# Kernel optimization log

Measured on AMD Instinct MI355X. Metric: run time of the kernel, lower is better.

The kernel has to match this reference:

```python
import jax, jax.numpy as jnp
import numpy as np

LN_EPS = 1e-5

def layer_norm(x, w, b):
    mu = jnp.mean(x, axis=-1, keepdims=True)
    var = jnp.mean(jnp.square(x - mu), axis=-1, keepdims=True)
    return (x - mu) * jax.lax.rsqrt(var + LN_EPS) * w + b

def setup_inputs() -> dict:
    key = jax.random.key(0)
    ks = jax.random.split(key, 8)
    B, F, Q, D = 8, 4096, 64, 1024
    H, DH = 16, 64
    inner = H * DH
    s = 1.0 / np.sqrt(D)
    return {
        "features": jax.random.normal(ks[0], (B, F, D), jnp.float32),
        "latents": jax.random.normal(ks[1], (B, Q, D), jnp.float32),
        "key_attention_mask": jax.random.randint(ks[2], (B, F), 0, 2, jnp.int32),
        "ln_m_w": jnp.ones((D,), jnp.float32),
        "ln_m_b": jnp.zeros((D,), jnp.float32),
        "ln_l_w": jnp.ones((D,), jnp.float32),
        "ln_l_b": jnp.zeros((D,), jnp.float32),
        "Wq": jax.random.normal(ks[3], (D, inner), jnp.float32) * s,
        "Wk": jax.random.normal(ks[4], (D, inner), jnp.float32) * s,
        "Wv": jax.random.normal(ks[5], (D, inner), jnp.float32) * s,
        "Wo": jax.random.normal(ks[6], (inner, D), jnp.float32) * (1.0 / np.sqrt(inner)),
    }

def reference(features, latents, key_attention_mask, ln_m_w, ln_m_b, ln_l_w, ln_l_b, Wq, Wk, Wv, Wo):
    H, DH = 16, 64
    B, F, D = features.shape
    Q = latents.shape[1]
    scale = DH ** (-0.5)

    x = layer_norm(features, ln_m_w, ln_m_b)          # [B,F,D]
    lat = layer_norm(latents, ln_l_w, ln_l_b)          # [B,Q,D]

    q = (lat @ Wq).reshape(B, Q, H, DH).transpose(0, 2, 1, 3)   # [B,H,Q,DH]
    kv_in = jnp.concatenate([x, lat], axis=1)                    # [B,F+Q,D]
    k = (kv_in @ Wk).reshape(B, F + Q, H, DH).transpose(0, 2, 1, 3)
    v = (kv_in @ Wv).reshape(B, F + Q, H, DH).transpose(0, 2, 1, 3)

    q = q * scale
    sim = jnp.einsum('bhqd,bhfd->bhqf', q, k)                    # [B,H,Q,F+Q]

    full_mask = jnp.concatenate(
        [key_attention_mask, jnp.ones((B, Q), key_attention_mask.dtype)], axis=1)  # [B,F+Q]
    sim = jnp.where(full_mask[:, None, None, :] == 0, -jnp.inf, sim)

    sim = sim - jax.lax.stop_gradient(jnp.max(sim, axis=-1, keepdims=True))
    alphas = jax.nn.softmax(sim, axis=-1)
    out = jnp.einsum('bhqf,bhfv->bhqv', alphas, v)               # [B,H,Q,DH]
    out = out.transpose(0, 2, 1, 3).reshape(B, Q, H * DH)        # [B,Q,inner]
    return out @ Wo                                              # [B,Q,D]
```

## Files before the change

### kernel.cpp

```cpp
#include <hip/hip_runtime.h>
#include <hip/hip_bf16.h>

#define B_    8
#define F_    4096
#define Qn    64
#define Dm    1024
#define Hh    16
#define DHn   64
#define FQ    4160
#define ROWS_KV 33280
#define ROWS_F  32768
#define KS    13
#define CHPB  5
#define KVOFF ((size_t)ROWS_KV * 1024)

typedef __bf16 v8bf __attribute__((ext_vector_type(8)));
typedef __bf16 v4bf __attribute__((ext_vector_type(4)));
typedef float  v4f  __attribute__((ext_vector_type(4)));

__device__ inline void gl_lds16(const __bf16* g, __bf16* l) {
  __builtin_amdgcn_global_load_lds((__attribute__((address_space(1))) void*)(g),
                                   (__attribute__((address_space(3))) void*)(l),
                                   16, 0, 0);
}

__device__ inline bool is_bf16_inputs(const void* mw) {
  return ((const unsigned int*)mw)[0] != 0x3F800000u;
}

__global__ __launch_bounds__(256) void transpose_kernel(
    const void* __restrict__ w0, const void* __restrict__ w1,
    const void* __restrict__ w2, const void* __restrict__ w3,
    __bf16* __restrict__ t0, __bf16* __restrict__ t1,
    __bf16* __restrict__ t2, __bf16* __restrict__ t3,
    const void* __restrict__ mw)
{
  bool bf = is_bf16_inputs(mw);
  __shared__ __bf16 tile[32][33];
  const void* src; __bf16* dst;
  switch (blockIdx.z) {
    case 0: src = w0; dst = t0; break;
    case 1: src = w1; dst = t1; break;
    case 2: src = w2; dst = t2; break;
    default: src = w3; dst = t3; break;
  }
  int tx = threadIdx.x, ty = threadIdx.y;
  int x = blockIdx.x * 32 + tx;
  #pragma unroll
  for (int j = 0; j < 4; ++j) {
    int y = blockIdx.y * 32 + ty + j * 8;
    size_t e = (size_t)y * 1024 + x;
    float v = bf ? (float)((const __bf16*)src)[e] : ((const float*)src)[e];
    tile[ty + j * 8][tx] = (__bf16)v;
  }
  __syncthreads();
  int x2 = blockIdx.y * 32 + tx;
  #pragma unroll
  for (int j = 0; j < 4; ++j) {
    int y2 = blockIdx.x * 32 + ty + j * 8;
    dst[(size_t)y2 * 1024 + x2] = tile[tx][ty + j * 8];
  }
}

__global__ __launch_bounds__(256) void ln_kernel(
    const void* __restrict__ feat, const void* __restrict__ lat,
    const void* __restrict__ mw, const void* __restrict__ mb,
    const void* __restrict__ lw, const void* __restrict__ lb,
    __bf16* __restrict__ kv_bf, __bf16* __restrict__ lat_bf)
{
  bool bf = is_bf16_inputs(mw);
  int tid = threadIdx.x;
  int wave = tid >> 6, lane = tid & 63;
  int r = blockIdx.x * 4 + wave;
  const void *rowp, *w, *g;
  __bf16 *dst, *dst2 = nullptr;
  size_t rowoff;
  if (r < ROWS_F) {
    rowoff = (size_t)r * Dm; rowp = feat; w = mw; g = mb;
    int b = r >> 12, f = r & (F_ - 1);
    dst = kv_bf + ((size_t)b * FQ + f) * Dm;
  } else {
    int r2 = r - ROWS_F;
    rowoff = (size_t)r2 * Dm; rowp = lat; w = lw; g = lb;
    int b = r2 >> 6, q = r2 & 63;
    dst  = kv_bf + ((size_t)b * FQ + F_ + q) * Dm;
    dst2 = lat_bf + (size_t)r2 * Dm;
  }
  float xs[16], ws_[16], gs[16];
  if (bf) {
    const __bf16* rp = (const __bf16*)rowp + rowoff;
    const __bf16* wp = (const __bf16*)w;
    const __bf16* gp = (const __bf16*)g;
    #pragma unroll
    for (int g2 = 0; g2 < 2; ++g2) {
      int base = g2 * 512 + lane * 8;
      v8bf X = *(const v8bf*)(rp + base);
      v8bf W = *(const v8bf*)(wp + base);
      v8bf G = *(const v8bf*)(gp + base);
      #pragma unroll
      for (int j = 0; j < 8; ++j) {
        xs[g2*8+j] = (float)X[j]; ws_[g2*8+j] = (float)W[j]; gs[g2*8+j] = (float)G[j];
      }
    }
  } else {
    const float* rp = (const float*)rowp + rowoff;
    const float* wp = (const float*)w;
    const float* gp = (const float*)g;
    #pragma unroll
    for (int g4 = 0; g4 < 4; ++g4) {
      int base = g4 * 256 + lane * 4;
      float4 X = *(const float4*)(rp + base);
      float4 W = *(const float4*)(wp + base);
      float4 G = *(const float4*)(gp + base);
      xs[g4*4]=X.x; xs[g4*4+1]=X.y; xs[g4*4+2]=X.z; xs[g4*4+3]=X.w;
      ws_[g4*4]=W.x; ws_[g4*4+1]=W.y; ws_[g4*4+2]=W.z; ws_[g4*4+3]=W.w;
      gs[g4*4]=G.x; gs[g4*4+1]=G.y; gs[g4*4+2]=G.z; gs[g4*4+3]=G.w;
    }
  }
  float s = 0.f, ss = 0.f;
  #pragma unroll
  for (int j = 0; j < 16; ++j) { s += xs[j]; ss += xs[j] * xs[j]; }
  #pragma unroll
  for (int off = 32; off > 0; off >>= 1) {
    s  += __shfl_xor(s, off, 64);
    ss += __shfl_xor(ss, off, 64);
  }
  float mean = s * (1.f / 1024.f);
  float var  = ss * (1.f / 1024.f) - mean * mean;
  float rs = rsqrtf(var + 1e-5f);
  float os[16];
  #pragma unroll
  for (int j = 0; j < 16; ++j) os[j] = (xs[j] - mean) * rs * ws_[j] + gs[j];
  if (bf) {
    #pragma unroll
    for (int g2 = 0; g2 < 2; ++g2) {
      int base = g2 * 512 + lane * 8;
      v8bf O;
      #pragma unroll
      for (int j = 0; j < 8; ++j) O[j] = (__bf16)os[g2*8+j];
      *(v8bf*)(dst + base) = O;
      if (dst2) *(v8bf*)(dst2 + base) = O;
    }
  } else {
    #pragma unroll
    for (int g4 = 0; g4 < 4; ++g4) {
      int base = g4 * 256 + lane * 4;
      v4bf O;
      #pragma unroll
      for (int j = 0; j < 4; ++j) O[j] = (__bf16)os[g4*4+j];
      *(v4bf*)(dst + base) = O;
      if (dst2) *(v4bf*)(dst2 + base) = O;
    }
  }
}


#define BAR() asm volatile("s_barrier" ::: "memory")

#define PH(Q) do { \
  BAR(); \
  asm volatile("s_waitcnt lgkmcnt(0)" ::: "memory"); \
  __builtin_amdgcn_s_setprio(1); \
  Q; \
  __builtin_amdgcn_s_setprio(0); \
  BAR(); \
} while (0)

#define PHV(Q) do { \
  BAR(); \
  asm volatile("s_waitcnt lgkmcnt(0)" ::: "memory"); \
  __builtin_amdgcn_s_setprio(1); \
  Q; \
  __builtin_amdgcn_s_setprio(0); \
  asm volatile("s_waitcnt vmcnt(4)" ::: "memory"); \
  BAR(); \
} while (0)

#define QUAD(MB, NB, BF) do { \
  _Pragma("unroll") \
  for (int m_ = 0; m_ < 4; ++m_) { \
    _Pragma("unroll") \
    for (int n_ = 0; n_ < 2; ++n_) { \
      _Pragma("unroll") \
      for (int k_ = 0; k_ < 2; ++k_) { \
        acc[(MB) + m_][(NB) + n_] = __builtin_amdgcn_mfma_f32_16x16x32_bf16( \
            af[m_][k_], BF[n_][k_], acc[(MB) + m_][(NB) + n_], 0, 0, 0); \
      } } } } while (0)

#define LDA8(BB, ROFF) do { \
  _Pragma("unroll") \
  for (int m_ = 0; m_ < 4; ++m_) { \
    _Pragma("unroll") \
    for (int k_ = 0; k_ < 2; ++k_) { \
      const int r_ = (ROFF) + m_ * 16 + lm; \
      af[m_][k_] = *(const v8bf*)(aB[BB] + ((r_ << 7) + ((k_ * 64 + kcb) ^ ((r_ & 7) << 4)))); \
    } } } while (0)

#define LDB4(BB, DST, NOFF) do { \
  _Pragma("unroll") \
  for (int n_ = 0; n_ < 2; ++n_) { \
    _Pragma("unroll") \
    for (int k_ = 0; k_ < 2; ++k_) { \
      const int r_ = bq + (NOFF) + n_ * 16 + lm; \
      DST[n_][k_] = *(const v8bf*)(bB[BB] + ((r_ << 7) + ((k_ * 64 + kcb) ^ ((r_ & 7) << 4)))); \
    } } } while (0)

#define STAGE_A(BB, H, K0) do { \
  gl_lds16(asrc + (size_t)(H) * 131072 + (K0),         (__bf16*)(ldsw + ((BB) * 4 + (H)) * 16384)); \
  gl_lds16(asrc + (size_t)(H) * 131072 + (K0) + 65536, (__bf16*)(ldsw + ((BB) * 4 + (H)) * 16384 + 8192)); \
} while (0)

#define STAGE_B(BB, H, K0) do { \
  gl_lds16(bsrc + (size_t)(H) * 131072 + (K0),         (__bf16*)(ldsw + ((BB) * 4 + 2 + (H)) * 16384)); \
  gl_lds16(bsrc + (size_t)(H) * 131072 + (K0) + 65536, (__bf16*)(ldsw + ((BB) * 4 + 2 + (H)) * 16384 + 8192)); \
} while (0)

__global__ __launch_bounds__(512, 2) void gemm_kv8_kernel(
    const __bf16* __restrict__ A, const __bf16* __restrict__ BtKV,
    __bf16* __restrict__ KVb)
{
  __shared__ __align__(16) char ldsm[131072];
  const int tid = threadIdx.x;
  const int lane = tid & 63, wave = tid >> 6;
  const int wm = wave >> 2, wn = wave & 3;
  const int lm = lane & 15, l4 = lane >> 4;
  const int kcb = l4 << 4;
  const int bq = (wn & 1) << 6;

  const int wg = (blockIdx.x & 7) * 130 + (blockIdx.x >> 3);
  const int n0 = (wg & 7) << 8;
  const int m0 = (wg >> 3) << 8;

  const int r0 = (wave << 3) + (lane >> 3);
  const int xc = ((lane & 7) ^ (lane >> 3)) << 3;
  const __bf16* asrc = A    + (size_t)(m0 + r0) * 1024 + xc;
  const __bf16* bsrc = BtKV + (size_t)(n0 + r0) * 1024 + xc;
  char* const ldsw = ldsm + tid * 16;
  const char* const aB[2] = { ldsm + wm * 16384, ldsm + (4 + wm) * 16384 };
  const char* const bB[2] = { ldsm + (2 + (wn >> 1)) * 16384,
                              ldsm + (6 + (wn >> 1)) * 16384 };

  v4f acc[8][4];
  #pragma unroll
  for (int i = 0; i < 8; ++i)
    #pragma unroll
    for (int j = 0; j < 4; ++j) acc[i][j] = (v4f){0.f, 0.f, 0.f, 0.f};
  v8bf af[4][2], blo[2][2], bhi[2][2];

  STAGE_A(0, 0, 0); STAGE_A(0, 1, 0);
  STAGE_B(0, 0, 0); STAGE_B(0, 1, 0);
  STAGE_B(1, 0, 64); STAGE_B(1, 1, 64);
  asm volatile("s_waitcnt vmcnt(4)" ::: "memory");
  BAR();

  #pragma unroll 1
  for (int it = 0; it < 8; ++it) {
    const int kA1 = (2 * it + 1) << 6;
    const int kT0 = (it < 7) ? ((2 * it + 2) << 6) : 0;
    const int kT1 = (it < 7) ? ((2 * it + 3) << 6) : 0;

    LDA8(0, 0); LDB4(0, blo, 0);
    STAGE_A(1, 0, kA1);
    PH(QUAD(0, 0, blo));

    LDB4(0, bhi, 32);
    STAGE_A(1, 1, kA1);
    PH(QUAD(0, 2, bhi));

    LDA8(0, 64);
    STAGE_B(0, 0, kT0);
    PH(QUAD(4, 2, bhi));

    STAGE_B(0, 1, kT0);
    PHV(QUAD(4, 0, blo));

    LDA8(1, 0); LDB4(1, blo, 0);
    STAGE_A(0, 0, kT0);
    PH(QUAD(0, 0, blo));

    LDB4(1, bhi, 32);
    STAGE_A(0, 1, kT0);
    PH(QUAD(0, 2, bhi));

    LDA8(1, 64);
    STAGE_B(1, 0, kT1);
    PH(QUAD(4, 2, bhi));

    STAGE_B(1, 1, kT1);
    PHV(QUAD(4, 0, blo));
  }

  const int cb = n0 + (wn << 6);
  const int rb = m0 + (wm << 7);
  #pragma unroll
  for (int m = 0; m < 8; ++m)
    #pragma unroll
    for (int n = 0; n < 4; ++n) {
      int col = cb + n * 16 + lm;
      int h = (col >> 6) & 15;
      int dh = col & 63;
      size_t vo = (col >= 1024) ? KVOFF : (size_t)0;
      #pragma unroll
      for (int reg = 0; reg < 4; ++reg) {
        int row = rb + m * 16 + l4 * 4 + reg;
        int bb2 = row / FQ; int f = row - bb2 * FQ;
        size_t idx = ((size_t)(bb2 * Hh + h) * FQ + f) * 64 + dh;
        KVb[idx + vo] = (__bf16)acc[m][n][reg];
      }
    }
}

__global__ __launch_bounds__(256) void gemm2_kernel(
    const __bf16* __restrict__ A, const __bf16* __restrict__ Bt,
    void* __restrict__ C, int mode, int out_follow,
    const void* __restrict__ mw)
{
  int obf = out_follow ? (is_bf16_inputs(mw) ? 1 : 0) : 1;

  __shared__ __align__(16) __bf16 As0[128 * 32];
  __shared__ __align__(16) __bf16 As1[128 * 32];
  __shared__ __align__(16) __bf16 Bs0[128 * 32];
  __shared__ __align__(16) __bf16 Bs1[128 * 32];
  int tid = threadIdx.x;
  int lane = tid & 63, wave = tid >> 6;
  int wm = wave >> 1, wn = wave & 1;
  int m0 = blockIdx.y * 128, n0 = blockIdx.x * 128;
  int lm = lane & 15, lk = (lane >> 4) << 3;

  v4f acc[4][4];
  #pragma unroll
  for (int i = 0; i < 4; ++i)
    #pragma unroll
    for (int j = 0; j < 4; ++j) acc[i][j] = (v4f){0.f, 0.f, 0.f, 0.f};

  int c0 = tid, c1 = tid + 256;
  const __bf16* a0p = A  + (size_t)(m0 + (c0 >> 2)) * 1024 + ((c0 & 3) << 3);
  const __bf16* a1p = A  + (size_t)(m0 + (c1 >> 2)) * 1024 + ((c1 & 3) << 3);
  const __bf16* b0p = Bt + (size_t)(n0 + (c0 >> 2)) * 1024 + ((c0 & 3) << 3);
  const __bf16* b1p = Bt + (size_t)(n0 + (c1 >> 2)) * 1024 + ((c1 & 3) << 3);

  for (int k0 = 0; k0 < 1024; k0 += 64) {
    __syncthreads();
    gl_lds16(a0p + k0,      &As0[c0 * 8]);
    gl_lds16(a1p + k0,      &As0[c1 * 8]);
    gl_lds16(a0p + k0 + 32, &As1[c0 * 8]);
    gl_lds16(a1p + k0 + 32, &As1[c1 * 8]);
    gl_lds16(b0p + k0,      &Bs0[c0 * 8]);
    gl_lds16(b1p + k0,      &Bs0[c1 * 8]);
    gl_lds16(b0p + k0 + 32, &Bs1[c0 * 8]);
    gl_lds16(b1p + k0 + 32, &Bs1[c1 * 8]);
    __syncthreads();
    {
      v8bf a[4], b[4];
      #pragma unroll
      for (int i = 0; i < 4; ++i) a[i] = *(const v8bf*)&As0[(wm * 64 + i * 16 + lm) * 32 + lk];
      #pragma unroll
      for (int j = 0; j < 4; ++j) b[j] = *(const v8bf*)&Bs0[(wn * 64 + j * 16 + lm) * 32 + lk];
      #pragma unroll
      for (int i = 0; i < 4; ++i)
        #pragma unroll
        for (int j = 0; j < 4; ++j)
          acc[i][j] = __builtin_amdgcn_mfma_f32_16x16x32_bf16(a[i], b[j], acc[i][j], 0, 0, 0);
    }
    {
      v8bf a[4], b[4];
      #pragma unroll
      for (int i = 0; i < 4; ++i) a[i] = *(const v8bf*)&As1[(wm * 64 + i * 16 + lm) * 32 + lk];
      #pragma unroll
      for (int j = 0; j < 4; ++j) b[j] = *(const v8bf*)&Bs1[(wn * 64 + j * 16 + lm) * 32 + lk];
      #pragma unroll
      for (int i = 0; i < 4; ++i)
        #pragma unroll
        for (int j = 0; j < 4; ++j)
          acc[i][j] = __builtin_amdgcn_mfma_f32_16x16x32_bf16(a[i], b[j], acc[i][j], 0, 0, 0);
    }
  }

  #pragma unroll
  for (int i = 0; i < 4; ++i)
    #pragma unroll
    for (int j = 0; j < 4; ++j) {
      int col = n0 + wn * 64 + j * 16 + lm;
      #pragma unroll
      for (int reg = 0; reg < 4; ++reg) {
        int row = m0 + wm * 64 + i * 16 + (lane >> 4) * 4 + reg;
        size_t idx;
        if (mode == 0) {
          idx = (size_t)row * 1024 + col;
        } else {
          int bb = row >> 6; int qq = row & 63;
          idx = ((size_t)(bb * Hh + (col >> 6)) * 64 + qq) * 64 + (col & 63);
        }
        float v = acc[i][j][reg];
        if (obf) ((__bf16*)C)[idx] = (__bf16)v;
        else     ((float*)C)[idx]  = v;
      }
    }
}

__global__ __launch_bounds__(256) void attn_part_kernel(
    const __bf16* __restrict__ Qm, const __bf16* __restrict__ K,
    const __bf16* __restrict__ V, const int* __restrict__ mask,
    float* __restrict__ Opart, float2* __restrict__ ml)
{
  __shared__ __align__(16) __bf16 qs[64 * 72];
  __shared__ __align__(16) __bf16 ks[64 * 72];
  __shared__ __align__(16) __bf16 vts[64 * 72];
  __shared__ __align__(16) __bf16 ps[64 * 72];
  __shared__ float msb[64];

  int tid = threadIdx.x;
  int lane = tid & 63, wave = tid >> 6;
  int ksb = blockIdx.x;
  int bh = blockIdx.y;
  int b = bh >> 4;
  int lm = lane & 15, lq = lane >> 4;

  const __bf16* qsrc = Qm + (size_t)bh * 64 * 64;
  #pragma unroll
  for (int i = 0; i < 2; ++i) {
    int e = (tid + 256 * i) * 8;
    int row = e >> 6, c = e & 63;
    *(v8bf*)&qs[row * 72 + c] = *(const v8bf*)(qsrc + e);
  }

  float mrow[4], lrow[4];
  v4f acco[4];
  #pragma unroll
  for (int r = 0; r < 4; ++r) { mrow[r] = -1e30f; lrow[r] = 0.f; }
  #pragma unroll
  for (int s = 0; s < 4; ++s) acco[s] = (v4f){0.f, 0.f, 0.f, 0.f};

  const __bf16* kbase = K + (size_t)bh * FQ * 64;
  const __bf16* vbase = V + (size_t)bh * FQ * 64;
  const int* maskb = mask + b * F_;

  for (int cc = 0; cc < CHPB; ++cc) {
    int chunk = ksb * CHPB + cc;
    __syncthreads();
    const __bf16* kc = kbase + (size_t)chunk * 4096;
    const __bf16* vc = vbase + (size_t)chunk * 4096;
    #pragma unroll
    for (int i = 0; i < 2; ++i) {
      int e = (tid + 256 * i) * 8;
      int row = e >> 6, c = e & 63;
      *(v8bf*)&ks[row * 72 + c] = *(const v8bf*)(kc + e);
      v8bf vv = *(const v8bf*)(vc + e);
      #pragma unroll
      for (int j = 0; j < 8; ++j) vts[(c + j) * 72 + row] = vv[j];
    }
    if (tid < 64) {
      int kidx = chunk * 64 + tid;
      msb[tid] = (kidx < F_) ? (maskb[kidx] != 0 ? 0.f : -1e30f) : 0.f;
    }
    __syncthreads();

    v8bf aq0 = *(const v8bf*)&qs[(wave * 16 + lm) * 72 + lq * 8];
    v8bf aq1 = *(const v8bf*)&qs[(wave * 16 + lm) * 72 + lq * 8 + 32];
    v4f sf[4];
    #pragma unroll
    for (int s = 0; s < 4; ++s) {
      v8bf bk0 = *(const v8bf*)&ks[(s * 16 + lm) * 72 + lq * 8];
      v8bf bk1 = *(const v8bf*)&ks[(s * 16 + lm) * 72 + lq * 8 + 32];
      v4f z = (v4f){0.f, 0.f, 0.f, 0.f};
      z = __builtin_amdgcn_mfma_f32_16x16x32_bf16(aq0, bk0, z, 0, 0, 0);
      z = __builtin_amdgcn_mfma_f32_16x16x32_bf16(aq1, bk1, z, 0, 0, 0);
      sf[s] = z;
    }
    float bias[4];
    #pragma unroll
    for (int s = 0; s < 4; ++s) bias[s] = msb[s * 16 + lm];
    #pragma unroll
    for (int s = 0; s < 4; ++s)
      #pragma unroll
      for (int r = 0; r < 4; ++r)
        sf[s][r] = sf[s][r] * 0.125f + bias[s];

    #pragma unroll
    for (int r = 0; r < 4; ++r) {
      float mx = fmaxf(fmaxf(sf[0][r], sf[1][r]), fmaxf(sf[2][r], sf[3][r]));
      #pragma unroll
      for (int off = 1; off < 16; off <<= 1) mx = fmaxf(mx, __shfl_xor(mx, off, 64));
      float mN = fmaxf(mrow[r], mx);
      float alpha = __expf(mrow[r] - mN);
      mrow[r] = mN;
      float ls = 0.f;
      #pragma unroll
      for (int s = 0; s < 4; ++s) { float p = __expf(sf[s][r] - mN); sf[s][r] = p; ls += p; }
      #pragma unroll
      for (int off = 1; off < 16; off <<= 1) ls += __shfl_xor(ls, off, 64);
      lrow[r] = lrow[r] * alpha + ls;
      #pragma unroll
      for (int s = 0; s < 4; ++s) acco[s][r] *= alpha;
    }

    #pragma unroll
    for (int s = 0; s < 4; ++s)
      #pragma unroll
      for (int r = 0; r < 4; ++r)
        ps[(wave * 16 + lq * 4 + r) * 72 + s * 16 + lm] = (__bf16)sf[s][r];

    v8bf ap0 = *(const v8bf*)&ps[(wave * 16 + lm) * 72 + lq * 8];
    v8bf ap1 = *(const v8bf*)&ps[(wave * 16 + lm) * 72 + lq * 8 + 32];
    #pragma unroll
    for (int s = 0; s < 4; ++s) {
      v8bf bv0 = *(const v8bf*)&vts[(s * 16 + lm) * 72 + lq * 8];
      v8bf bv1 = *(const v8bf*)&vts[(s * 16 + lm) * 72 + lq * 8 + 32];
      acco[s] = __builtin_amdgcn_mfma_f32_16x16x32_bf16(ap0, bv0, acco[s], 0, 0, 0);
      acco[s] = __builtin_amdgcn_mfma_f32_16x16x32_bf16(ap1, bv1, acco[s], 0, 0, 0);
    }
  }

  float* Ob = Opart + (((size_t)ksb * 128 + bh) * 64) * 64;
  #pragma unroll
  for (int s = 0; s < 4; ++s)
    #pragma unroll
    for (int r = 0; r < 4; ++r) {
      int q = wave * 16 + lq * 4 + r;
      Ob[q * 64 + s * 16 + lm] = acco[s][r];
    }
  if (lm == 0) {
    #pragma unroll
    for (int r = 0; r < 4; ++r) {
      int q = wave * 16 + lq * 4 + r;
      ml[((size_t)ksb * 128 + bh) * 64 + q] = make_float2(mrow[r], lrow[r]);
    }
  }
}

__global__ __launch_bounds__(256) void attn_comb_kernel(
    const float* __restrict__ Opart, const float2* __restrict__ ml,
    __bf16* __restrict__ attnb)
{
  int bh = blockIdx.x;
  int b = bh >> 4, h = bh & 15;
  int t = threadIdx.x;
  int q = t >> 2, cg = (t & 3) * 16;

  float m_[KS], l_[KS];
  float M = -1e30f;
  #pragma unroll
  for (int k = 0; k < KS; ++k) {
    float2 p = ml[((size_t)k * 128 + bh) * 64 + q];
    m_[k] = p.x; l_[k] = p.y;
    M = fmaxf(M, p.x);
  }
  float L = 0.f;
  #pragma unroll
  for (int k = 0; k < KS; ++k) L += l_[k] * __expf(m_[k] - M);
  float o[16];
  #pragma unroll
  for (int j = 0; j < 16; ++j) o[j] = 0.f;
  #pragma unroll
  for (int k = 0; k < KS; ++k) {
    float wgt = __expf(m_[k] - M);
    const float* P = Opart + ((((size_t)k * 128 + bh) * 64 + q) * 64) + cg;
    #pragma unroll
    for (int j4 = 0; j4 < 4; ++j4) {
      float4 pv = *(const float4*)(P + j4 * 4);
      o[j4*4]   += pv.x * wgt; o[j4*4+1] += pv.y * wgt;
      o[j4*4+2] += pv.z * wgt; o[j4*4+3] += pv.w * wgt;
    }
  }
  float invL = 1.f / L;
  __bf16* dst = attnb + ((size_t)(b * 64 + q) * 1024) + h * 64 + cg;
  v8bf O0, O1;
  #pragma unroll
  for (int j = 0; j < 8; ++j) { O0[j] = (__bf16)(o[j] * invL); O1[j] = (__bf16)(o[8+j] * invL); }
  *(v8bf*)dst = O0;
  *(v8bf*)(dst + 8) = O1;
}

extern "C" void kernel_launch(void* const* d_in, const int* in_sizes, int n_in,
                              void* d_out, int out_size, void* d_ws, size_t ws_size,
                              hipStream_t stream)
{
  void* feat = d_in[0];
  void* lat  = d_in[1];
  const int* mk = (const int*)d_in[2];
  void* mw = d_in[3]; void* mb = d_in[4];
  void* lw = d_in[5]; void* lb = d_in[6];
  void* Wq = d_in[7]; void* Wk = d_in[8];
  void* Wv = d_in[9]; void* Wo = d_in[10];

  char* ws = (char*)d_ws;
  size_t off = 0;
  auto alloc = [&](size_t bytes) {
    char* p = ws + off;
    off += (bytes + 255) & ~(size_t)255;
    return p;
  };
  __bf16* WkvT  = (__bf16*)alloc((size_t)2 * 1024 * 1024 * 2);
  __bf16* WqT   = (__bf16*)alloc((size_t)1024 * 1024 * 2);
  __bf16* WoT   = (__bf16*)alloc((size_t)1024 * 1024 * 2);
  __bf16* KVb   = (__bf16*)alloc((size_t)2 * ROWS_KV * 1024 * 2);
  __bf16* Qmb   = (__bf16*)alloc((size_t)512 * 1024 * 2);
  __bf16* attnb = (__bf16*)alloc((size_t)512 * 1024 * 2);
  __bf16* lat_bf= (__bf16*)alloc((size_t)512 * 1024 * 2);
  char*   big   = (char*)alloc((size_t)ROWS_KV * 1024 * 2);
  __bf16* kv_bf = (__bf16*)big;
  float*  Opart = (float*)big;
  float2* ml    = (float2*)(big + (size_t)KS*128*64*64*4);
  if (ws_size < off) return;

  transpose_kernel<<<dim3(32, 32, 4), dim3(32, 8), 0, stream>>>(
      Wq, Wk, Wv, Wo, WqT, WkvT, WkvT + (size_t)1024 * 1024, WoT, mw);

  ln_kernel<<<8320, 256, 0, stream>>>(feat, lat, mw, mb, lw, lb, kv_bf, lat_bf);

  gemm_kv8_kernel<<<dim3(1040), dim3(512), 0, stream>>>(kv_bf, WkvT, KVb);
  gemm2_kernel<<<dim3(8, 4), 256, 0, stream>>>(lat_bf, WqT, Qmb, 2, 0, mw);

  attn_part_kernel<<<dim3(KS, 128), 256, 0, stream>>>(
      Qmb, KVb, KVb + KVOFF, mk, Opart, ml);
  attn_comb_kernel<<<128, 256, 0, stream>>>(Opart, ml, attnb);

  gemm2_kernel<<<dim3(8, 4), 256, 0, stream>>>(attnb, WoT, d_out, 0, 1, mw);
}
```

Before: 489.6 us.

## Fuse Q projection into KV GEMM, stage epilogue via LDS, store V transposed

Merges the Q projection GEMM into the big KV GEMM by appending 8 extra workgroups that read the latent rows against a combined WkvT+WqT weight buffer, removing one launch. The KV epilogue now stages the accumulator tile through swizzled LDS and writes 16-byte vector stores instead of scattered 2-byte stores. V is written in a transposed [bh, dh, f] layout so the attention kernel loads it with vector loads rather than doing an element-wise LDS transpose. This adds LDS round trips and extra barriers in the epilogue.

```diff
diff --git a/kernel.cpp b/kernel.cpp
--- a/kernel.cpp
+++ b/kernel.cpp
@@ -216,8 +216,9 @@
 } while (0)
 
 __global__ __launch_bounds__(512, 2) void gemm_kv8_kernel(
-    const __bf16* __restrict__ A, const __bf16* __restrict__ BtKV,
-    __bf16* __restrict__ KVb)
+    const __bf16* __restrict__ A, const __bf16* __restrict__ lat,
+    const __bf16* __restrict__ BtKV,
+    __bf16* __restrict__ KVb, __bf16* __restrict__ Qmb)
 {
   __shared__ __align__(16) char ldsm[131072];
   const int tid = threadIdx.x;
@@ -227,13 +228,15 @@
   const int kcb = l4 << 4;
   const int bq = (wn & 1) << 6;
 
-  const int wg = (blockIdx.x & 7) * 130 + (blockIdx.x >> 3);
-  const int n0 = (wg & 7) << 8;
-  const int m0 = (wg >> 3) << 8;
+  const int wg = (blockIdx.x & 7) * 131 + (blockIdx.x >> 3);
+  int m0, n0;
+  const __bf16* abase;
+  if (wg < 1040) { m0 = (wg >> 3) << 8; n0 = (wg & 7) << 8; abase = A; }
+  else { int qb = wg - 1040; m0 = (qb >> 2) << 8; n0 = 2048 + ((qb & 3) << 8); abase = lat; }
 
   const int r0 = (wave << 3) + (lane >> 3);
   const int xc = ((lane & 7) ^ (lane >> 3)) << 3;
-  const __bf16* asrc = A    + (size_t)(m0 + r0) * 1024 + xc;
+  const __bf16* asrc = abase + (size_t)(m0 + r0) * 1024 + xc;
   const __bf16* bsrc = BtKV + (size_t)(n0 + r0) * 1024 + xc;
   char* const ldsw = ldsm + tid * 16;
   const char* const aB[2] = { ldsm + wm * 16384, ldsm + (4 + wm) * 16384 };
@@ -290,24 +293,81 @@
     PHV(QUAD(4, 0, blo));
   }
 
-  const int cb = n0 + (wn << 6);
-  const int rb = m0 + (wm << 7);
-  #pragma unroll
-  for (int m = 0; m < 8; ++m)
-    #pragma unroll
-    for (int n = 0; n < 4; ++n) {
-      int col = cb + n * 16 + lm;
-      int h = (col >> 6) & 15;
-      int dh = col & 63;
-      size_t vo = (col >= 1024) ? KVOFF : (size_t)0;
-      #pragma unroll
-      for (int reg = 0; reg < 4; ++reg) {
-        int row = rb + m * 16 + l4 * 4 + reg;
-        int bb2 = row / FQ; int f = row - bb2 * FQ;
-        size_t idx = ((size_t)(bb2 * Hh + h) * FQ + f) * 64 + dh;
-        KVb[idx + vo] = (__bf16)acc[m][n][reg];
+  const int rb_l = wm << 7;
+  const int cb_l = wn << 6;
+
+  if (n0 >= 2048) {
+    #pragma unroll
+    for (int m = 0; m < 8; ++m)
+      #pragma unroll
+      for (int n = 0; n < 4; ++n) {
+        int col = n0 + cb_l + n * 16 + lm;
+        int h = (col >> 6) & 15, dh = col & 63;
+        #pragma unroll
+        for (int reg = 0; reg < 4; ++reg) {
+          int row = m0 + rb_l + m * 16 + l4 * 4 + reg;
+          int b = row >> 6, q = row & 63;
+          Qmb[((size_t)(b * Hh + h) * 64 + q) * 64 + dh] = (__bf16)acc[m][n][reg];
+        }
       }
-    }
+  } else if (n0 >= 1024) {
+    __syncthreads();
+    #pragma unroll
+    for (int m = 0; m < 8; ++m)
+      #pragma unroll
+      for (int n = 0; n < 4; ++n)
+        #pragma unroll
+        for (int reg = 0; reg < 4; ++reg) {
+          int rl = rb_l + m * 16 + l4 * 4 + reg;
+          int cl = cb_l + n * 16 + lm;
+          int byt = (cl << 9) + ((rl << 1) ^ (((cl >> 2) & 7) << 5));
+          *(__bf16*)(ldsm + byt) = (__bf16)acc[m][n][reg];
+        }
+    __syncthreads();
+    {
+      const int g = tid >> 4, s = tid & 15;
+      #pragma unroll
+      for (int p = 0; p < 16; ++p) {
+        int d = p * 32 + g;
+        int cl = d >> 1, hf = d & 1;
+        int byt = (cl << 9) + ((((hf << 8) + (s << 4))) ^ (((cl >> 2) & 7) << 5));
+        v8bf val = *(const v8bf*)(ldsm + byt);
+        int col = n0 + cl;
+        int h = (col >> 6) & 15, dh = col & 63;
+        int row = m0 + (hf << 7) + (s << 3);
+        int b = row / FQ, f = row - b * FQ;
+        *(v8bf*)(KVb + KVOFF + ((size_t)(b * Hh + h) * 64 + dh) * FQ + f) = val;
+      }
+    }
+  } else {
+    __syncthreads();
+    #pragma unroll
+    for (int m = 0; m < 8; ++m)
+      #pragma unroll
+      for (int n = 0; n < 4; ++n)
+        #pragma unroll
+        for (int reg = 0; reg < 4; ++reg) {
+          int rl = rb_l + m * 16 + l4 * 4 + reg;
+          int cl = cb_l + n * 16 + lm;
+          int byt = (rl << 9) + ((cl << 1) ^ (((rl >> 2) & 7) << 5));
+          *(__bf16*)(ldsm + byt) = (__bf16)acc[m][n][reg];
+        }
+    __syncthreads();
+    {
+      const int g = tid >> 3, s = tid & 7;
+      #pragma unroll
+      for (int p = 0; p < 16; ++p) {
+        int d = p * 64 + g;
+        int hl = d >> 8, fl = d & 255;
+        int byt = (fl << 9) + ((((hl << 7) + (s << 4))) ^ (((fl >> 2) & 7) << 5));
+        v8bf val = *(const v8bf*)(ldsm + byt);
+        int row = m0 + fl;
+        int b = row / FQ, f = row - b * FQ;
+        int h = ((n0 + (hl << 6)) >> 6) & 15;
+        *(v8bf*)(KVb + ((size_t)(b * Hh + h) * FQ + f) * 64 + (s << 3)) = val;
+      }
+    }
+  }
 }
 
 __global__ __launch_bounds__(256) void gemm2_kernel(
@@ -400,7 +460,7 @@
 
 __global__ __launch_bounds__(256) void attn_part_kernel(
     const __bf16* __restrict__ Qm, const __bf16* __restrict__ K,
-    const __bf16* __restrict__ V, const int* __restrict__ mask,
+    const __bf16* __restrict__ Vt, const int* __restrict__ mask,
     float* __restrict__ Opart, float2* __restrict__ ml)
 {
   __shared__ __align__(16) __bf16 qs[64 * 72];
@@ -432,22 +492,20 @@
   for (int s = 0; s < 4; ++s) acco[s] = (v4f){0.f, 0.f, 0.f, 0.f};
 
   const __bf16* kbase = K + (size_t)bh * FQ * 64;
-  const __bf16* vbase = V + (size_t)bh * FQ * 64;
+  const __bf16* vbase = Vt + (size_t)bh * 64 * FQ;
   const int* maskb = mask + b * F_;
 
   for (int cc = 0; cc < CHPB; ++cc) {
     int chunk = ksb * CHPB + cc;
     __syncthreads();
     const __bf16* kc = kbase + (size_t)chunk * 4096;
-    const __bf16* vc = vbase + (size_t)chunk * 4096;
+    const __bf16* vc = vbase + chunk * 64;
     #pragma unroll
     for (int i = 0; i < 2; ++i) {
       int e = (tid + 256 * i) * 8;
       int row = e >> 6, c = e & 63;
-      *(v8bf*)&ks[row * 72 + c] = *(const v8bf*)(kc + e);
-      v8bf vv = *(const v8bf*)(vc + e);
-      #pragma unroll
-      for (int j = 0; j < 8; ++j) vts[(c + j) * 72 + row] = vv[j];
+      *(v8bf*)&ks[row * 72 + c]  = *(const v8bf*)(kc + e);
+      *(v8bf*)&vts[row * 72 + c] = *(const v8bf*)(vc + (size_t)row * FQ + c);
     }
     if (tid < 64) {
       int kidx = chunk * 64 + tid;
@@ -590,8 +648,7 @@
     off += (bytes + 255) & ~(size_t)255;
     return p;
   };
-  __bf16* WkvT  = (__bf16*)alloc((size_t)2 * 1024 * 1024 * 2);
-  __bf16* WqT   = (__bf16*)alloc((size_t)1024 * 1024 * 2);
+  __bf16* WkvT  = (__bf16*)alloc((size_t)3 * 1024 * 1024 * 2);
   __bf16* WoT   = (__bf16*)alloc((size_t)1024 * 1024 * 2);
   __bf16* KVb   = (__bf16*)alloc((size_t)2 * ROWS_KV * 1024 * 2);
   __bf16* Qmb   = (__bf16*)alloc((size_t)512 * 1024 * 2);
@@ -604,12 +661,16 @@
   if (ws_size < off) return;
 
   transpose_kernel<<<dim3(32, 32, 4), dim3(32, 8), 0, stream>>>(
-      Wq, Wk, Wv, Wo, WqT, WkvT, WkvT + (size_t)1024 * 1024, WoT, mw);
+      Wq, Wk, Wv, Wo,
+      WkvT + (size_t)2 * 1024 * 1024,
+      WkvT,
+      WkvT + (size_t)1024 * 1024,
+      WoT, mw);
 
   ln_kernel<<<8320, 256, 0, stream>>>(feat, lat, mw, mb, lw, lb, kv_bf, lat_bf);
 
-  gemm_kv8_kernel<<<dim3(1040), dim3(512), 0, stream>>>(kv_bf, WkvT, KVb);
-  gemm2_kernel<<<dim3(8, 4), 256, 0, stream>>>(lat_bf, WqT, Qmb, 2, 0, mw);
+  gemm_kv8_kernel<<<dim3(1048), dim3(512), 0, stream>>>(
+      kv_bf, lat_bf, WkvT, KVb, Qmb);
 
   attn_part_kernel<<<dim3(KS, 128), 256, 0, stream>>>(
       Qmb, KVb, KVb + KVOFF, mk, Opart, ml);
```

New measurement: 450.5 us. -8.0%, faster.
